# Kernel optimization log

Hardware: AMD Instinct MI355X
Metric: run time of the kernel (lower is better)

Reference implementation:

```python
import jax, jax.numpy as jnp
import numpy as np

EMBED, HEADS, LEVELS, POINTS, FFN = 256, 8, 4, 4, 1024
HD = EMBED // HEADS


def layer_norm(x, g, b, eps=1e-5):
    m = jnp.mean(x, axis=-1, keepdims=True)
    v = jnp.mean((x - m) ** 2, axis=-1, keepdims=True)
    return (x - m) / jnp.sqrt(v + eps) * g + b


def ms_deform_attn_core(value, shapes_np, loc, attn):
    # value: (B, nk, H, hd); loc: (B, nq, H, L, P, 2) normalized [0,1]; attn: (B, nq, H, L, P)
    B, nq = loc.shape[0], loc.shape[1]
    splits = np.cumsum(shapes_np[:, 0] * shapes_np[:, 1])[:-1]
    vals = jnp.split(value, splits, axis=1)
    out = jnp.zeros((B, HEADS, nq, HD), value.dtype)
    for l in range(LEVELS):
        Hl, Wl = int(shapes_np[l, 0]), int(shapes_np[l, 1])
        v = vals[l].transpose(0, 2, 1, 3)                     # (B, H, Hl*Wl, hd)
        x = loc[:, :, :, l, :, 0] * Wl - 0.5                  # (B, nq, H, P) pixel coords
        y = loc[:, :, :, l, :, 1] * Hl - 0.5
        x0 = jnp.floor(x); y0 = jnp.floor(y)
        fx = x - x0; fy = y - y0
        x0i = x0.astype(jnp.int32); y0i = y0.astype(jnp.int32)
        acc = jnp.zeros((B, HEADS, nq * POINTS, HD), value.dtype)
        for dx, dy, w in ((0, 0, (1 - fx) * (1 - fy)), (1, 0, fx * (1 - fy)),
                          (0, 1, (1 - fx) * fy), (1, 1, fx * fy)):
            xi = x0i + dx; yi = y0i + dy
            valid = (xi >= 0) & (xi < Wl) & (yi >= 0) & (yi < Hl)
            idx = jnp.clip(yi, 0, Hl - 1) * Wl + jnp.clip(xi, 0, Wl - 1)  # (B, nq, H, P)
            idx_f = idx.transpose(0, 2, 1, 3).reshape(B, HEADS, -1)
            g = jnp.take_along_axis(v, idx_f[..., None], axis=2)          # (B, H, nq*P, hd)
            wv = jnp.where(valid, w, 0.0).transpose(0, 2, 1, 3).reshape(B, HEADS, -1, 1)
            acc = acc + g * wv
        aw = attn[:, :, :, l].transpose(0, 2, 1, 3).reshape(B, HEADS, -1, 1)
        out = out + (acc * aw).reshape(B, HEADS, nq, POINTS, HD).sum(3)
    return out.transpose(0, 2, 1, 3).reshape(B, nq, EMBED)


def setup_inputs() -> dict:
    key = jax.random.key(0)
    ks = jax.random.split(key, 20)
    B = 2
    shapes = np.array([[136, 136], [68, 68], [34, 34], [17, 17]], np.int32)
    nk = int((shapes[:, 0] * shapes[:, 1]).sum())  # 24565
    lsi = np.concatenate([[0], np.cumsum(shapes[:, 0] * shapes[:, 1])[:-1]]).astype(np.int32)

    def lin(k, i, o):
        return jax.random.normal(k, (i, o), jnp.float32) * 0.02

    return {
        "src": jax.random.normal(ks[0], (B, nk, EMBED), jnp.float32),
        "reference_points": jax.random.uniform(ks[1], (B, nk, LEVELS, 2), jnp.float32),
        "spatial_shapes": jnp.asarray(shapes),
        "level_start_index": jnp.asarray(lsi),
        "w_off": lin(ks[2], EMBED, HEADS * LEVELS * POINTS * 2),
        "b_off": jax.random.normal(ks[3], (HEADS * LEVELS * POINTS * 2,), jnp.float32) * 0.5,
        "w_att": lin(ks[4], EMBED, HEADS * LEVELS * POINTS),
        "b_att": jnp.zeros((HEADS * LEVELS * POINTS,), jnp.float32),
        "w_val": lin(ks[5], EMBED, EMBED), "b_val": jnp.zeros((EMBED,), jnp.float32),
        "w_out": lin(ks[6], EMBED, EMBED), "b_out": jnp.zeros((EMBED,), jnp.float32),
        "g1": jnp.ones((EMBED,), jnp.float32), "bt1": jnp.zeros((EMBED,), jnp.float32),
        "w1": lin(ks[7], EMBED, FFN), "b1": jnp.zeros((FFN,), jnp.float32),
        "w2": lin(ks[8], FFN, EMBED), "b2": jnp.zeros((EMBED,), jnp.float32),
        "g2": jnp.ones((EMBED,), jnp.float32), "bt2": jnp.zeros((EMBED,), jnp.float32),
    }


def reference(src, reference_points, spatial_shapes, level_start_index,
              w_off, b_off, w_att, b_att, w_val, b_val, w_out, b_out,
              g1, bt1, w1, b1, w2, b2, g2, bt2):
    B, nq, D = src.shape
    shapes_np = np.asarray(spatial_shapes)
    # projections
    value = (src @ w_val + b_val).reshape(B, nq, HEADS, HD)
    off = (src @ w_off + b_off).reshape(B, nq, HEADS, LEVELS, POINTS, 2)
    attn = (src @ w_att + b_att).reshape(B, nq, HEADS, LEVELS * POINTS)
    attn = jax.nn.softmax(attn, axis=-1).reshape(B, nq, HEADS, LEVELS, POINTS)
    # sampling locations: ref + offset / [W, H] per level
    normalizer = jnp.asarray(shapes_np[:, ::-1].copy(), src.dtype)  # (L, 2) = [W, H]
    loc = reference_points[:, :, None, :, None, :] + off / normalizer[None, None, None, :, None, :]
    attn_out = ms_deform_attn_core(value, shapes_np, loc, attn) @ w_out + b_out
    x = layer_norm(src + attn_out, g1, bt1)
    ffn = jax.nn.relu(x @ w1 + b1) @ w2 + b2
    return layer_norm(x + ffn, g2, bt2)
```

## Files before the change

### kernel.cpp

```cpp
#include <hip/hip_runtime.h>
#include <math.h>

#define EMBED 256
#define HEADS 8
#define LEVELS 4
#define POINTS 4
#define FFNDIM 1024

typedef float f32x4 __attribute__((ext_vector_type(4)));
typedef float f32x2 __attribute__((ext_vector_type(2)));
typedef __bf16 bf16x8 __attribute__((ext_vector_type(8)));

static __device__ __forceinline__ float4 ld4f(const float* p) {
    return *reinterpret_cast<const float4*>(p);
}
static __device__ __forceinline__ unsigned short f2bf(float f) {
    unsigned int u = __float_as_uint(f);
    unsigned int r = (u + 0x7fffu + ((u >> 16) & 1u)) >> 16;
    return (unsigned short)r;
}
static __device__ __forceinline__ float bf2f(unsigned short u) {
    return __uint_as_float((unsigned int)u << 16);
}
static __device__ __forceinline__ f32x2 pkfma(f32x2 a, f32x2 b, f32x2 c) {
#if __has_builtin(__builtin_elementwise_fma)
    return __builtin_elementwise_fma(a, b, c);
#else
    f32x2 r; r.x = fmaf(a.x, b.x, c.x); r.y = fmaf(a.y, b.y, c.y); return r;
#endif
}
static __device__ __forceinline__
void gl_lds16(const unsigned short* g, unsigned short* l) {
    __builtin_amdgcn_global_load_lds(
        (const __attribute__((address_space(1))) unsigned int*)g,
        (__attribute__((address_space(3))) unsigned int*)l, 16, 0, 0);
}

__global__ __launch_bounds__(256)
void k_cvt_src(const float* __restrict__ src, unsigned short* __restrict__ dst, int n)
{
    int i = (blockIdx.x * 256 + threadIdx.x) * 4;
    const int stride = gridDim.x * 1024;
    for (; i < n; i += stride) {
        float4 v = ld4f(src + i);
        ushort4 o;
        o.x = f2bf(v.x); o.y = f2bf(v.y); o.z = f2bf(v.z); o.w = f2bf(v.w);
        *reinterpret_cast<ushort4*>(dst + i) = o;
    }
}

__global__ __launch_bounds__(256)
void k_cvt_w(const float* __restrict__ wv, const float* __restrict__ wo,
             const float* __restrict__ wa, const float* __restrict__ wout,
             const float* __restrict__ w1, const float* __restrict__ w2,
             unsigned short* __restrict__ wcat, unsigned short* __restrict__ woutt,
             unsigned short* __restrict__ w1t, unsigned short* __restrict__ w2t)
{
    const int total = 163840 + 65536 + 262144 + 262144;
    for (int gid = blockIdx.x * 256 + threadIdx.x; gid < total; gid += gridDim.x * 256) {
        int local = gid;
        float f; unsigned short* dst;
        if (local < 163840) {
            int n = local >> 8, k = local & 255;
            if (n < 256)      f = wv[k * 256 + n];
            else if (n < 512) f = wo[k * 256 + (n - 256)];
            else              f = wa[k * 128 + (n - 512)];
            dst = wcat + local;
        } else if ((local -= 163840) < 65536) {
            int n = local >> 8, k = local & 255;
            f = wout[k * 256 + n];
            dst = woutt + local;
        } else if ((local -= 65536) < 262144) {
            int n = local >> 8, k = local & 255;
            f = w1[k * 1024 + n];
            dst = w1t + local;
        } else {
            local -= 262144;
            int n = local >> 10, k = local & 1023;
            f = w2[k * 256 + n];
            dst = w2t + local;
        }
        *dst = f2bf(f);
    }
}


#define GEMM_STAGE(Aptr, ASTR, Wptr, WSTR, kcexp)                              \
    {                                                                          \
        int row = (wid << 3) + (lane >> 3);                                    \
        int slot = (lane & 7) ^ (row & 7);                                     \
        gl_lds16(Aptr + (size_t)(m0 + row) * ASTR + (kcexp) * 64 + slot * 8,   \
                 a_s + (size_t)(wid << 3) * 64);                               \
    }                                                                          \
    _Pragma("unroll")                                                          \
    for (int rnd = 0; rnd < 4; ++rnd) {                                        \
        int row = (rnd << 6) + (wid << 3) + (lane >> 3);                       \
        int slot = (lane & 7) ^ (row & 7);                                     \
        gl_lds16(Wptr + (size_t)(n0 + row) * WSTR + (kcexp) * 64 + slot * 8,   \
                 w_s + (size_t)((rnd << 6) + (wid << 3)) * 64);                \
    }

#define GEMM_FRAGS_MFMA                                                        \
    {                                                                          \
        bf16x8 af[2][2], bfr[4][2];                                            \
        const int ksb = (lane >> 4);                                           \
        _Pragma("unroll")                                                      \
        for (int i = 0; i < 2; ++i) {                                          \
            int m = wm * 32 + i * 16 + cl;                                     \
            _Pragma("unroll")                                                  \
            for (int kk = 0; kk < 2; ++kk) {                                   \
                int phys = (kk * 4 + ksb) ^ (m & 7);                           \
                af[i][kk] = *reinterpret_cast<const bf16x8*>(                  \
                    a_s + m * 64 + phys * 8);                                  \
            }                                                                  \
        }                                                                      \
        _Pragma("unroll")                                                      \
        for (int j = 0; j < 4; ++j) {                                          \
            int n = wn * 64 + j * 16 + cl;                                     \
            _Pragma("unroll")                                                  \
            for (int kk = 0; kk < 2; ++kk) {                                   \
                int phys = (kk * 4 + ksb) ^ (n & 7);                           \
                bfr[j][kk] = *reinterpret_cast<const bf16x8*>(                 \
                    w_s + n * 64 + phys * 8);                                  \
            }                                                                  \
        }                                                                      \
        _Pragma("unroll")                                                      \
        for (int kk = 0; kk < 2; ++kk)                                         \
            _Pragma("unroll")                                                  \
            for (int i = 0; i < 2; ++i)                                        \
                _Pragma("unroll")                                              \
                for (int j = 0; j < 4; ++j)                                    \
                    acc[i][j] = __builtin_amdgcn_mfma_f32_16x16x32_bf16(       \
                        af[i][kk], bfr[j][kk], acc[i][j], 0, 0, 0);            \
    }

__global__ __launch_bounds__(512)
void k_proj(const unsigned short* __restrict__ A, const unsigned short* __restrict__ Wt,
            const float* __restrict__ b_val, const float* __restrict__ b_off,
            const float* __restrict__ b_att,
            unsigned short* __restrict__ value, unsigned short* __restrict__ offr,
            unsigned short* __restrict__ attw, int M)
{
    __shared__ __align__(16) unsigned short smem[20480];
    unsigned short* a_s = smem;
    unsigned short* w_s = smem + 4096;
    const int tid = threadIdx.x;
    const int m0 = blockIdx.x * 64;
    const int y = blockIdx.y;
    const int n0 = y * 256;
    const int lane = tid & 63, wid = tid >> 6;
    const int wm = wid >> 2, wn = wid & 3;
    const int cl = lane & 15, r4 = (lane >> 4) * 4;

    f32x4 acc[2][4] = {};

    for (int kc = 0; kc < 4; ++kc) {
        __syncthreads();
        GEMM_STAGE(A, 256, Wt, 256, kc)
        __syncthreads();
        GEMM_FRAGS_MFMA
    }

    if (y < 2) {
        unsigned short* dst = (y == 0) ? value : offr;
        const float* bias = (y == 0) ? b_val : b_off;
        __syncthreads();
        #pragma unroll
        for (int j = 0; j < 4; ++j) {
            int col = wn * 64 + j * 16 + cl;
            float bv = bias[col];
            #pragma unroll
            for (int i = 0; i < 2; ++i)
                #pragma unroll
                for (int r = 0; r < 4; ++r)
                    smem[(wm * 32 + i * 16 + r4 + r) * 264 + col] = f2bf(acc[i][j][r] + bv);
        }
        __syncthreads();
        #pragma unroll
        for (int t = 0; t < 4; ++t) {
            int idx = tid + t * 512;
            int row = idx >> 5, cu = idx & 31;
            int grow = m0 + row;
            if (grow < M)
                *reinterpret_cast<uint4*>(dst + (size_t)grow * 256 + cu * 8) =
                    *reinterpret_cast<const uint4*>(smem + row * 264 + cu * 8);
        }
    } else {
        if (wn < 2) {
            #pragma unroll
            for (int j = 0; j < 4; ++j) {
                int a = wn * 64 + j * 16 + cl;
                float bv = b_att[a];
                #pragma unroll
                for (int i = 0; i < 2; ++i) {
                    #pragma unroll
                    for (int r = 0; r < 4; ++r) {
                        float v = acc[i][j][r] + bv;
                        float mx = v;
                        mx = fmaxf(mx, __shfl_xor(mx, 1));
                        mx = fmaxf(mx, __shfl_xor(mx, 2));
                        mx = fmaxf(mx, __shfl_xor(mx, 4));
                        mx = fmaxf(mx, __shfl_xor(mx, 8));
                        float e = __expf(v - mx);
                        float s = e;
                        s += __shfl_xor(s, 1);
                        s += __shfl_xor(s, 2);
                        s += __shfl_xor(s, 4);
                        s += __shfl_xor(s, 8);
                        acc[i][j][r] = e / s;
                    }
                }
            }
        }
        __syncthreads();
        if (wn < 2) {
            #pragma unroll
            for (int j = 0; j < 4; ++j) {
                int a = wn * 64 + j * 16 + cl;
                #pragma unroll
                for (int i = 0; i < 2; ++i)
                    #pragma unroll
                    for (int r = 0; r < 4; ++r)
                        smem[(wm * 32 + i * 16 + r4 + r) * 136 + a] = f2bf(acc[i][j][r]);
            }
        }
        __syncthreads();
        #pragma unroll
        for (int t = 0; t < 2; ++t) {
            int idx = tid + t * 512;
            int row = idx >> 4, cu = idx & 15;
            int grow = m0 + row;
            if (grow < M)
                *reinterpret_cast<uint4*>(attw + (size_t)grow * 128 + cu * 8) =
                    *reinterpret_cast<const uint4*>(smem + row * 136 + cu * 8);
        }
    }
}

__global__ __launch_bounds__(256)
void k_sample(const unsigned short* __restrict__ value,
              const unsigned short* __restrict__ offr,
              const unsigned short* __restrict__ attw,
              const float* __restrict__ ref,
              const int* __restrict__ shapes, const int* __restrict__ lsi,
              unsigned short* __restrict__ core, int M)
{
    __shared__ int2 iw_s[8][8][65];
    const int tid = threadIdx.x;
    const int tok0 = blockIdx.x * 8;
    const int nk = lsi[3] + shapes[6] * shapes[7];

    #pragma unroll
    for (int q = 0; q < 4; ++q) {
        const int task = tid + q * 256;
        const int tl = task >> 7;
        const int rest = task & 127;
        const int l = (rest >> 2) & 3;
        const int lp = rest & 15;
        const int hh = rest >> 4;
        const int tok = tok0 + tl;
        int2 out[4];
        if (tok < M) {
            const int Hl = shapes[l * 2], Wl = shapes[l * 2 + 1];
            const int base = ((tok >= nk) ? nk : 0) + lsi[l];
            const float rx = ref[(size_t)tok * 8 + l * 2];
            const float ry = ref[(size_t)tok * 8 + l * 2 + 1];
            const unsigned int oxy =
                *reinterpret_cast<const unsigned int*>(offr + (size_t)tok * 256 + rest * 2);
            const float ox = bf2f((unsigned short)(oxy & 0xffffu));
            const float oy = bf2f((unsigned short)(oxy >> 16));
            const float aw = bf2f(attw[(size_t)tok * 128 + rest]);
            const float x = fmaf(rx, (float)Wl, ox) - 0.5f;
            const float y = fmaf(ry, (float)Hl, oy) - 0.5f;
            const float x0f = floorf(x), y0f = floorf(y);
            const float fx = x - x0f, fy = y - y0f;
            const int x0 = (int)x0f, y0 = (int)y0f;
            #pragma unroll
            for (int t = 0; t < 4; ++t) {
                const int dx = t & 1, dy = t >> 1;
                const int xi = x0 + dx, yi = y0 + dy;
                const bool valid = (xi >= 0) & (xi < Wl) & (yi >= 0) & (yi < Hl);
                const float w = (dx ? fx : 1.f - fx) * (dy ? fy : 1.f - fy) * aw;
                const int xc = min(max(xi, 0), Wl - 1);
                const int yc = min(max(yi, 0), Hl - 1);
                out[t].x = (base + yc * Wl + xc) * 128;
                out[t].y = __float_as_int(valid ? w : 0.f);
            }
        } else {
            #pragma unroll
            for (int t = 0; t < 4; ++t) out[t] = make_int2(0, 0);
        }
        #pragma unroll
        for (int t = 0; t < 4; ++t)
            iw_s[tl][hh][lp * 4 + t] = out[t];
    }
    __syncthreads();

    const int tl = tid >> 5;
    const int h = (tid >> 2) & 7;
    const int dp = tid & 3;
    const int tok = tok0 + tl;
    const unsigned int* vu = reinterpret_cast<const unsigned int*>(value);
    const int choff = h * 16 + dp * 4;
    const int2* pt = &iw_s[tl][h][0];
    f32x2 a0 = {0.f, 0.f}, a1 = {0.f, 0.f};
    f32x2 a2 = {0.f, 0.f}, a3 = {0.f, 0.f};
    #pragma unroll 16
    for (int q = 0; q < 64; ++q) {
        const int2 iw = pt[q];
        const float w = __int_as_float(iw.y);
        const f32x2 w2 = {w, w};
        const uint4 v = *reinterpret_cast<const uint4*>(vu + (size_t)(unsigned)iw.x + choff);
        const f32x2 v0 = {__uint_as_float(v.x << 16), __uint_as_float(v.x & 0xffff0000u)};
        const f32x2 v1 = {__uint_as_float(v.y << 16), __uint_as_float(v.y & 0xffff0000u)};
        const f32x2 v2 = {__uint_as_float(v.z << 16), __uint_as_float(v.z & 0xffff0000u)};
        const f32x2 v3 = {__uint_as_float(v.w << 16), __uint_as_float(v.w & 0xffff0000u)};
        a0 = pkfma(v0, w2, a0);
        a1 = pkfma(v1, w2, a1);
        a2 = pkfma(v2, w2, a2);
        a3 = pkfma(v3, w2, a3);
    }
    if (tok < M) {
        uint4 o;
        o.x = (unsigned int)f2bf(a0.x) | ((unsigned int)f2bf(a0.y) << 16);
        o.y = (unsigned int)f2bf(a1.x) | ((unsigned int)f2bf(a1.y) << 16);
        o.z = (unsigned int)f2bf(a2.x) | ((unsigned int)f2bf(a2.y) << 16);
        o.w = (unsigned int)f2bf(a3.x) | ((unsigned int)f2bf(a3.y) << 16);
        *reinterpret_cast<uint4*>(core + (size_t)tok * 256 + choff * 2) = o;
    }
}

__global__ __launch_bounds__(512)
void k_oproj(const unsigned short* __restrict__ A, const unsigned short* __restrict__ Wt,
             const float* __restrict__ b_out, const float* __restrict__ src,
             const float* __restrict__ g1, const float* __restrict__ bt1,
             unsigned short* __restrict__ X, int M)
{
    __shared__ __align__(16) unsigned short smem[20480];
    unsigned short* a_s = smem;
    unsigned short* w_s = smem + 4096;
    __shared__ float red[64 * 8];
    __shared__ float mr[64 * 2];
    const int tid = threadIdx.x;
    const int m0 = blockIdx.x * 64;
    const int n0 = 0;
    const int lane = tid & 63, wid = tid >> 6;
    const int wm = wid >> 2, wn = wid & 3;
    const int cl = lane & 15, r4 = (lane >> 4) * 4;

    f32x4 acc[2][4] = {};

    for (int kc = 0; kc < 4; ++kc) {
        __syncthreads();
        GEMM_STAGE(A, 256, Wt, 256, kc)
        __syncthreads();
        GEMM_FRAGS_MFMA
    }

    #pragma unroll
    for (int j = 0; j < 4; ++j) {
        int col = wn * 64 + j * 16 + cl;
        float bv = b_out[col];
        #pragma unroll
        for (int i = 0; i < 2; ++i) {
            int mb = wm * 32 + i * 16 + r4;
            #pragma unroll
            for (int r = 0; r < 4; ++r) {
                int row = m0 + mb + r;
                float sv = (row < M) ? src[(size_t)row * 256 + col] : 0.f;
                acc[i][j][r] += bv + sv;
            }
        }
    }
    #pragma unroll
    for (int i = 0; i < 2; ++i)
        #pragma unroll
        for (int r = 0; r < 4; ++r) {
            float s1 = 0.f, s2 = 0.f;
            #pragma unroll
            for (int j = 0; j < 4; ++j) { float t = acc[i][j][r]; s1 += t; s2 += t * t; }
            s1 += __shfl_xor(s1, 1); s2 += __shfl_xor(s2, 1);
            s1 += __shfl_xor(s1, 2); s2 += __shfl_xor(s2, 2);
            s1 += __shfl_xor(s1, 4); s2 += __shfl_xor(s2, 4);
            s1 += __shfl_xor(s1, 8); s2 += __shfl_xor(s2, 8);
            if (cl == 0) {
                int rr = wm * 32 + i * 16 + r4 + r;
                red[(rr * 4 + wn) * 2 + 0] = s1;
                red[(rr * 4 + wn) * 2 + 1] = s2;
            }
        }
    __syncthreads();
    if (tid < 64) {
        float s1 = red[tid * 8] + red[tid * 8 + 2] + red[tid * 8 + 4] + red[tid * 8 + 6];
        float s2 = red[tid * 8 + 1] + red[tid * 8 + 3] + red[tid * 8 + 5] + red[tid * 8 + 7];
        float mu = s1 * (1.f / 256.f);
        mr[tid * 2] = mu;
        mr[tid * 2 + 1] = rsqrtf(fmaxf(s2 * (1.f / 256.f) - mu * mu, 0.f) + 1e-5f);
    }
    __syncthreads();
    #pragma unroll
    for (int j = 0; j < 4; ++j) {
        int col = wn * 64 + j * 16 + cl;
        float gv = g1[col], bt = bt1[col];
        #pragma unroll
        for (int i = 0; i < 2; ++i)
            #pragma unroll
            for (int r = 0; r < 4; ++r) {
                int rr = wm * 32 + i * 16 + r4 + r;
                smem[rr * 264 + col] =
                    f2bf((acc[i][j][r] - mr[rr * 2]) * mr[rr * 2 + 1] * gv + bt);
            }
    }
    __syncthreads();
    #pragma unroll
    for (int t = 0; t < 4; ++t) {
        int idx = tid + t * 512;
        int row = idx >> 5, cu = idx & 31;
        int grow = m0 + row;
        if (grow < M)
            *reinterpret_cast<uint4*>(X + (size_t)grow * 256 + cu * 8) =
                *reinterpret_cast<const uint4*>(smem + row * 264 + cu * 8);
    }
}

__global__ __launch_bounds__(512)
void k_ffn1(const unsigned short* __restrict__ A, const unsigned short* __restrict__ W1t,
            const float* __restrict__ B1, unsigned short* __restrict__ h, int M)
{
    __shared__ __align__(16) unsigned short smem[20480];
    unsigned short* a_s = smem;
    unsigned short* w_s = smem + 4096;
    const int tid = threadIdx.x;
    const int m0 = blockIdx.x * 64;
    const int n0 = blockIdx.y * 256;
    const int lane = tid & 63, wid = tid >> 6;
    const int wm = wid >> 2, wn = wid & 3;
    const int cl = lane & 15, r4 = (lane >> 4) * 4;

    f32x4 acc[2][4] = {};

    for (int kc = 0; kc < 4; ++kc) {
        __syncthreads();
        GEMM_STAGE(A, 256, W1t, 256, kc)
        __syncthreads();
        GEMM_FRAGS_MFMA
    }

    __syncthreads();
    #pragma unroll
    for (int j = 0; j < 4; ++j) {
        int col = wn * 64 + j * 16 + cl;
        float bv = B1[n0 + col];
        #pragma unroll
        for (int i = 0; i < 2; ++i)
            #pragma unroll
            for (int r = 0; r < 4; ++r)
                smem[(wm * 32 + i * 16 + r4 + r) * 264 + col] =
                    f2bf(fmaxf(acc[i][j][r] + bv, 0.f));
    }
    __syncthreads();
    #pragma unroll
    for (int t = 0; t < 4; ++t) {
        int idx = tid + t * 512;
        int row = idx >> 5, cu = idx & 31;
        int grow = m0 + row;
        if (grow < M)
            *reinterpret_cast<uint4*>(h + (size_t)grow * 1024 + n0 + cu * 8) =
                *reinterpret_cast<const uint4*>(smem + row * 264 + cu * 8);
    }
}

__global__ __launch_bounds__(512)
void k_ffn2(const unsigned short* __restrict__ h, const unsigned short* __restrict__ W2t,
            const float* __restrict__ B2, const unsigned short* __restrict__ Xbf,
            const float* __restrict__ G2, const float* __restrict__ BT2,
            float* __restrict__ OUT, int M)
{
    __shared__ __align__(16) unsigned short smem[20480];
    unsigned short* a_s = smem;
    unsigned short* w_s = smem + 4096;
    __shared__ float red[64 * 8];
    __shared__ float mr[64 * 2];
    const int tid = threadIdx.x;
    const int m0 = blockIdx.x * 64;
    const int n0 = 0;
    const int lane = tid & 63, wid = tid >> 6;
    const int wm = wid >> 2, wn = wid & 3;
    const int cl = lane & 15, r4 = (lane >> 4) * 4;

    f32x4 acc[2][4] = {};

    for (int kc = 0; kc < 16; ++kc) {
        __syncthreads();
        GEMM_STAGE(h, 1024, W2t, 1024, kc)
        __syncthreads();
        GEMM_FRAGS_MFMA
    }

    #pragma unroll
    for (int j = 0; j < 4; ++j) {
        int col = wn * 64 + j * 16 + cl;
        float bv = B2[col];
        #pragma unroll
        for (int i = 0; i < 2; ++i) {
            int mb = wm * 32 + i * 16 + r4;
            #pragma unroll
            for (int r = 0; r < 4; ++r) {
                int row = m0 + mb + r;
                float xv = (row < M) ? bf2f(Xbf[(size_t)row * 256 + col]) : 0.f;
                acc[i][j][r] += bv + xv;
            }
        }
    }
    #pragma unroll
    for (int i = 0; i < 2; ++i)
        #pragma unroll
        for (int r = 0; r < 4; ++r) {
            float s1 = 0.f, s2 = 0.f;
            #pragma unroll
            for (int j = 0; j < 4; ++j) { float t = acc[i][j][r]; s1 += t; s2 += t * t; }
            s1 += __shfl_xor(s1, 1); s2 += __shfl_xor(s2, 1);
            s1 += __shfl_xor(s1, 2); s2 += __shfl_xor(s2, 2);
            s1 += __shfl_xor(s1, 4); s2 += __shfl_xor(s2, 4);
            s1 += __shfl_xor(s1, 8); s2 += __shfl_xor(s2, 8);
            if (cl == 0) {
                int rr = wm * 32 + i * 16 + r4 + r;
                red[(rr * 4 + wn) * 2 + 0] = s1;
                red[(rr * 4 + wn) * 2 + 1] = s2;
            }
        }
    __syncthreads();
    if (tid < 64) {
        float s1 = red[tid * 8] + red[tid * 8 + 2] + red[tid * 8 + 4] + red[tid * 8 + 6];
        float s2 = red[tid * 8 + 1] + red[tid * 8 + 3] + red[tid * 8 + 5] + red[tid * 8 + 7];
        float mu = s1 * (1.f / 256.f);
        mr[tid * 2] = mu;
        mr[tid * 2 + 1] = rsqrtf(fmaxf(s2 * (1.f / 256.f) - mu * mu, 0.f) + 1e-5f);
    }
    __syncthreads();
    #pragma unroll
    for (int j = 0; j < 4; ++j) {
        int col = wn * 64 + j * 16 + cl;
        float gv = G2[col], bt = BT2[col];
        #pragma unroll
        for (int i = 0; i < 2; ++i) {
            int mb = wm * 32 + i * 16 + r4;
            #pragma unroll
            for (int r = 0; r < 4; ++r) {
                int rr = mb + r, row = m0 + rr;
                if (row < M)
                    OUT[(size_t)row * 256 + col] =
                        (acc[i][j][r] - mr[rr * 2]) * mr[rr * 2 + 1] * gv + bt;
            }
        }
    }
}

extern "C" void kernel_launch(void* const* d_in, const int* in_sizes, int n_in,
                              void* d_out, int out_size, void* d_ws, size_t ws_size,
                              hipStream_t stream) {
    const float* src    = (const float*)d_in[0];
    const float* ref    = (const float*)d_in[1];
    const int*   shapes = (const int*)d_in[2];
    const int*   lsi    = (const int*)d_in[3];
    const float* b_off  = (const float*)d_in[5];
    const float* b_att  = (const float*)d_in[7];
    const float* b_val  = (const float*)d_in[9];
    const float* b_out  = (const float*)d_in[11];
    const float* g1     = (const float*)d_in[12];
    const float* bt1    = (const float*)d_in[13];
    const float* b1     = (const float*)d_in[15];
    const float* b2     = (const float*)d_in[17];
    const float* g2     = (const float*)d_in[18];
    const float* bt2    = (const float*)d_in[19];
    const float* w_off  = (const float*)d_in[4];
    const float* w_att  = (const float*)d_in[6];
    const float* w_val  = (const float*)d_in[8];
    const float* w_out  = (const float*)d_in[10];
    const float* w1     = (const float*)d_in[14];
    const float* w2     = (const float*)d_in[16];

    const int M = in_sizes[0] / EMBED;
    const size_t M256 = (size_t)M * 256;

    unsigned short* w16     = (unsigned short*)d_ws;
    unsigned short* src_bf  = w16;
    unsigned short* value_bf = src_bf + M256;
    unsigned short* offr_bf = value_bf + M256;
    unsigned short* core_bf = offr_bf + M256;
    unsigned short* x_bf    = core_bf + M256;
    unsigned short* attw_bf = x_bf + M256;
    unsigned short* wcat    = attw_bf + (size_t)M * 128;
    unsigned short* woutt   = wcat + 163840;
    unsigned short* w1t     = woutt + 65536;
    unsigned short* w2t     = w1t + 262144;
    unsigned short* h_bf    = w16;

    const int gb64 = (M + 63) / 64;
    const int gbS = (M + 7) / 8;

    k_cvt_src<<<4096, 256, 0, stream>>>(src, src_bf, M * 256);
    k_cvt_w<<<2944, 256, 0, stream>>>(w_val, w_off, w_att, w_out, w1, w2,
                                      wcat, woutt, w1t, w2t);
    k_proj<<<dim3(gb64, 3), 512, 0, stream>>>(src_bf, wcat, b_val, b_off, b_att,
                                              value_bf, offr_bf, attw_bf, M);
    k_sample<<<gbS, 256, 0, stream>>>(value_bf, offr_bf, attw_bf, ref, shapes, lsi,
                                      core_bf, M);
    k_oproj<<<gb64, 512, 0, stream>>>(core_bf, woutt, b_out, src, g1, bt1, x_bf, M);
    k_ffn1<<<dim3(gb64, 4), 512, 0, stream>>>(x_bf, w1t, b1, h_bf, M);
    k_ffn2<<<gb64, 512, 0, stream>>>(h_bf, w2t, b2, x_bf, g2, bt2,
                                     (float*)d_out, M);
}
```

Baseline: 277.1 us.

## Store value tensor head-major (B,H,nk,hd) to localize deformable sampling gathers

The value projection now writes its output in a per-batch, per-head contiguous layout instead of token-major with all heads interleaved. The sampling kernel computes gather indices against this layout, so each head's bilinear taps read from a compact 64-byte-per-pixel region, which should improve cache-line and L2 locality for the random gathers. The projection epilogue's global stores become scattered across head planes, and the host derives nk as M/2, which assumes two batches of equal size.

Result: no change. 280.0 us (+1.0%).

```diff
diff --git a/kernel.cpp b/kernel.cpp
--- a/kernel.cpp
+++ b/kernel.cpp
@@ -139,7 +139,7 @@
             const float* __restrict__ b_val, const float* __restrict__ b_off,
             const float* __restrict__ b_att,
             unsigned short* __restrict__ value, unsigned short* __restrict__ offr,
-            unsigned short* __restrict__ attw, int M)
+            unsigned short* __restrict__ attw, int M, int nk)
 {
     __shared__ __align__(16) unsigned short smem[20480];
     unsigned short* a_s = smem;
@@ -162,7 +162,6 @@
     }
 
     if (y < 2) {
-        unsigned short* dst = (y == 0) ? value : offr;
         const float* bias = (y == 0) ? b_val : b_off;
         __syncthreads();
         #pragma unroll
@@ -176,14 +175,31 @@
                     smem[(wm * 32 + i * 16 + r4 + r) * 264 + col] = f2bf(acc[i][j][r] + bv);
         }
         __syncthreads();
-        #pragma unroll
-        for (int t = 0; t < 4; ++t) {
-            int idx = tid + t * 512;
-            int row = idx >> 5, cu = idx & 31;
-            int grow = m0 + row;
-            if (grow < M)
-                *reinterpret_cast<uint4*>(dst + (size_t)grow * 256 + cu * 8) =
-                    *reinterpret_cast<const uint4*>(smem + row * 264 + cu * 8);
+        if (y == 0) {
+            #pragma unroll
+            for (int t = 0; t < 4; ++t) {
+                int idx = tid + t * 512;
+                int row = idx >> 5, cu = idx & 31;
+                int grow = m0 + row;
+                if (grow < M) {
+                    int b = grow >= nk;
+                    int pix = grow - (b ? nk : 0);
+                    int hh = cu >> 2, ch = (cu & 3) * 8;
+                    *reinterpret_cast<uint4*>(
+                        value + ((size_t)(b * 8 + hh) * nk + pix) * 32 + ch) =
+                        *reinterpret_cast<const uint4*>(smem + row * 264 + cu * 8);
+                }
+            }
+        } else {
+            #pragma unroll
+            for (int t = 0; t < 4; ++t) {
+                int idx = tid + t * 512;
+                int row = idx >> 5, cu = idx & 31;
+                int grow = m0 + row;
+                if (grow < M)
+                    *reinterpret_cast<uint4*>(offr + (size_t)grow * 256 + cu * 8) =
+                        *reinterpret_cast<const uint4*>(smem + row * 264 + cu * 8);
+            }
         }
     } else {
         if (wn < 2) {
@@ -262,7 +278,8 @@
         int2 out[4];
         if (tok < M) {
             const int Hl = shapes[l * 2], Wl = shapes[l * 2 + 1];
-            const int base = ((tok >= nk) ? nk : 0) + lsi[l];
+            const int bh = ((tok >= nk) ? 8 : 0) + hh;
+            const int pbase = bh * nk + lsi[l];
             const float rx = ref[(size_t)tok * 8 + l * 2];
             const float ry = ref[(size_t)tok * 8 + l * 2 + 1];
             const unsigned int oxy =
@@ -283,7 +300,7 @@
                 const float w = (dx ? fx : 1.f - fx) * (dy ? fy : 1.f - fy) * aw;
                 const int xc = min(max(xi, 0), Wl - 1);
                 const int yc = min(max(yi, 0), Hl - 1);
-                out[t].x = (base + yc * Wl + xc) * 128;
+                out[t].x = (pbase + yc * Wl + xc) * 16;
                 out[t].y = __float_as_int(valid ? w : 0.f);
             }
         } else {
@@ -300,8 +317,7 @@
     const int h = (tid >> 2) & 7;
     const int dp = tid & 3;
     const int tok = tok0 + tl;
-    const unsigned int* vu = reinterpret_cast<const unsigned int*>(value);
-    const int choff = h * 16 + dp * 4;
+    const unsigned int* vu = reinterpret_cast<const unsigned int*>(value) + dp * 4;
     const int2* pt = &iw_s[tl][h][0];
     f32x2 a0 = {0.f, 0.f}, a1 = {0.f, 0.f};
     f32x2 a2 = {0.f, 0.f}, a3 = {0.f, 0.f};
@@ -310,7 +326,7 @@
         const int2 iw = pt[q];
         const float w = __int_as_float(iw.y);
         const f32x2 w2 = {w, w};
-        const uint4 v = *reinterpret_cast<const uint4*>(vu + (size_t)(unsigned)iw.x + choff);
+        const uint4 v = *reinterpret_cast<const uint4*>(vu + (size_t)(unsigned)iw.x);
         const f32x2 v0 = {__uint_as_float(v.x << 16), __uint_as_float(v.x & 0xffff0000u)};
         const f32x2 v1 = {__uint_as_float(v.y << 16), __uint_as_float(v.y & 0xffff0000u)};
         const f32x2 v2 = {__uint_as_float(v.z << 16), __uint_as_float(v.z & 0xffff0000u)};
@@ -326,7 +342,7 @@
         o.y = (unsigned int)f2bf(a1.x) | ((unsigned int)f2bf(a1.y) << 16);
         o.z = (unsigned int)f2bf(a2.x) | ((unsigned int)f2bf(a2.y) << 16);
         o.w = (unsigned int)f2bf(a3.x) | ((unsigned int)f2bf(a3.y) << 16);
-        *reinterpret_cast<uint4*>(core + (size_t)tok * 256 + choff * 2) = o;
+        *reinterpret_cast<uint4*>(core + (size_t)tok * 256 + h * 32 + dp * 8) = o;
     }
 }
 
@@ -581,6 +597,7 @@
     const float* w2     = (const float*)d_in[16];
 
     const int M = in_sizes[0] / EMBED;
+    const int nk = M / 2;
     const size_t M256 = (size_t)M * 256;
 
     unsigned short* w16     = (unsigned short*)d_ws;
@@ -603,7 +620,7 @@
     k_cvt_w<<<2944, 256, 0, stream>>>(w_val, w_off, w_att, w_out, w1, w2,
                                       wcat, woutt, w1t, w2t);
     k_proj<<<dim3(gb64, 3), 512, 0, stream>>>(src_bf, wcat, b_val, b_off, b_att,
-                                              value_bf, offr_bf, attw_bf, M);
+                                              value_bf, offr_bf, attw_bf, M, nk);
     k_sample<<<gbS, 256, 0, stream>>>(value_bf, offr_bf, attw_bf, ref, shapes, lsi,
                                       core_bf, M);
     k_oproj<<<gb64, 512, 0, stream>>>(core_bf, woutt, b_out, src, g1, bt1, x_bf, M);
```
